# Performance work log

Hardware: AMD Instinct MI355X
Metric: run time of the kernel (lower is better)

The kernel has to match this reference:

```python
import jax, jax.numpy as jnp
import numpy as np

NH = 8  # num_heads


def setup_inputs() -> dict:
    key = jax.random.key(0)
    ks = jax.random.split(key, 6)
    B, H, W, M, C = 4, 32, 32, 21, 32  # M = 1^2 + 2^2 + 4^2 (window_sizes)
    B_ = B * H * W
    hd = C // NH
    s = lambda k, sh: jax.random.normal(k, sh, dtype=jnp.float32) * 0.02
    return {
        'x': jax.random.normal(ks[0], (B_, M, C), dtype=jnp.float32),
        'W_qkv': s(ks[1], (C, 3 * C)),
        'b_qkv': jnp.zeros((3 * C,), jnp.float32),
        'W_proj': s(ks[2], (C, C)),
        'b_proj': jnp.zeros((C,), jnp.float32),
        'W_sq': s(ks[3], (M * hd, 1)),
        'b_sq': jnp.zeros((1,), jnp.float32),
        'W_dw': s(ks[4], (2 * NH, 1, 3, 3)),  # depthwise conv, 2 outputs per head
        'b_dw': jnp.zeros((2 * NH,), jnp.float32),
        'batch_size': B,
        'H': H,
        'W': W,
    }


def reference(x, W_qkv, b_qkv, W_proj, b_proj, W_sq, b_sq, W_dw, b_dw, batch_size, H, W):
    B_, M, C = x.shape
    nh = NH
    hd = C // nh
    N = B_ // batch_size  # = H * W

    # qkv: (B_, M, 3C) -> (3, B, nh, N, M*hd)
    qkv = (x @ W_qkv + b_qkv).reshape(batch_size, N, M, 3, nh, hd)
    qkv = jnp.transpose(qkv, (3, 0, 4, 1, 2, 5)).reshape(3, batch_size, nh, N, M * hd)
    q, k, v = qkv[0], qkv[1], qkv[2]

    scale = N ** -0.5  # qk_scale=None -> (B_//batch_size)**-0.5
    attn = jnp.einsum('bhnd,bhmd->bhnm', q * scale, k)  # (B, nh, N, N)

    # ---- LSPE dynamic relative-position bias ----
    x2 = x.reshape(batch_size, H, W, M, nh, hd)
    x2 = jnp.transpose(x2, (0, 4, 1, 2, 3, 5)).reshape(batch_size, nh, H, W, M * hd)
    x2 = (x2 @ W_sq)[..., 0] + b_sq[0]  # (B, nh, H, W)

    conv = jax.lax.conv_general_dilated(
        x2, W_dw, (1, 1), [(1, 1), (1, 1)],
        dimension_numbers=('NCHW', 'OIHW', 'NCHW'), feature_group_count=nh)
    conv = conv + b_dw[None, :, None, None]  # (B, 2*nh, H, W)

    avg = jnp.mean(x2, axis=(2, 3), keepdims=True)  # adaptive avg pool to 1x1
    mx = jnp.max(x2, axis=(2, 3), keepdims=True)    # adaptive max pool to 1x1
    pooled = jnp.tile(avg + mx, (1, 2, H, W))       # torch .repeat(1,2,H,W)

    y = (conv + pooled).reshape(batch_size, 2, nh, H, W)
    y = jnp.transpose(y, (1, 0, 2, 3, 4))  # (2, B, nh, H, W)
    x_weight = jnp.mean(y[0], axis=0)[:, None]  # (nh, 1, H, W)
    x_proj = jnp.mean(y[1], axis=0)[None]       # (1, nh, H, W)

    # conv_transpose2d(stride=1, pad=0, groups=nh) == full correlation with flipped kernel
    bias = jax.lax.conv_general_dilated(
        x_proj, jnp.flip(x_weight, (-2, -1)), (1, 1),
        [(H - 1, H - 1), (W - 1, W - 1)],
        dimension_numbers=('NCHW', 'OIHW', 'NCHW'), feature_group_count=nh)
    table = bias[0].reshape(nh, -1).T  # ((2H-1)(2W-1), nh)

    coords = jnp.stack(jnp.meshgrid(jnp.arange(H), jnp.arange(W), indexing='ij'))
    coords = coords.reshape(2, -1)                     # (2, N)
    rel = coords[:, :, None] - coords[:, None, :]      # (2, N, N)
    idx = (rel[0] + H - 1) * (2 * W - 1) + (rel[1] + W - 1)  # (N, N)
    rel_bias = jnp.transpose(table[idx], (2, 0, 1))    # (nh, N, N)

    attn = jax.nn.softmax(attn + rel_bias[None], axis=-1)

    out = jnp.einsum('bhnm,bhmd->bhnd', attn, v)       # (B, nh, N, M*hd)
    out = jnp.transpose(out, (0, 2, 1, 3)).reshape(B_, nh, M, hd)
    out = jnp.transpose(out, (0, 2, 1, 3)).reshape(B_, M, C)
    return out @ W_proj + b_proj
```

## Files before the change

kernel.cpp:

```cpp
#include <hip/hip_runtime.h>
#include <math.h>

#define NHEAD 8
#define BATCH 4
#define NN 1024
#define MM 21
#define DD 84
#define DP 96
#define BN (BATCH*NHEAD)
#define NROWS (BATCH*NN*MM)

typedef __attribute__((ext_vector_type(8))) short bf16x8;
typedef __attribute__((ext_vector_type(16))) float f32x16;

__device__ __forceinline__ unsigned short f2bf(float x) {
    union { float f; unsigned int u; } c; c.f = x;
    unsigned int r = (c.u + 0x7FFFu + ((c.u >> 16) & 1u)) >> 16;
    return (unsigned short)r;
}
__device__ __forceinline__ int qxmap(int r, int half) { return (r & 3) + 8*(r >> 2) + 4*half; }


__global__ __launch_bounds__(256)
void qkv_kernel(const float* __restrict__ x, const float* __restrict__ Wq,
                const float* __restrict__ bq, ushort* __restrict__ qf,
                ushort* __restrict__ kf, ushort* __restrict__ vb)
{
    __shared__ ushort wqs[3072];
    __shared__ float bqs[96];
    __shared__ __align__(16) float xs[128*36];
    __shared__ ushort cs[4*3200];
    int t = threadIdx.x;
    int w = t >> 6, lane = t & 63, col = lane & 31, half = lane >> 5;
    int R0 = blockIdx.x * 128;

    for (int i = t; i < 3072; i += 256) wqs[i] = f2bf(Wq[i]);
    if (t < 96) bqs[t] = bq[t];
    for (int i = t; i < 4096; i += 256)
        xs[(i >> 5)*36 + (i & 31)] = x[(size_t)R0*32 + i];
    __syncthreads();

    bf16x8 bw[3][2];
#pragma unroll
    for (int f = 0; f < 3; f++)
#pragma unroll
        for (int c = 0; c < 2; c++) {
            union { bf16x8 v; ushort s[8]; } u;
#pragma unroll
            for (int j = 0; j < 8; j++)
                u.s[j] = wqs[(c*16 + half*8 + j)*96 + f*32 + col];
            bw[f][c] = u.v;
        }
    bf16x8 aw[2];
#pragma unroll
    for (int c = 0; c < 2; c++) {
        const float* xr = xs + (w*32 + col)*36 + c*16 + half*8;
        float4 v0 = *(const float4*)(xr);
        float4 v1 = *(const float4*)(xr + 4);
        union { bf16x8 v; ushort s[8]; } u;
        u.s[0]=f2bf(v0.x); u.s[1]=f2bf(v0.y); u.s[2]=f2bf(v0.z); u.s[3]=f2bf(v0.w);
        u.s[4]=f2bf(v1.x); u.s[5]=f2bf(v1.y); u.s[6]=f2bf(v1.z); u.s[7]=f2bf(v1.w);
        aw[c] = u.v;
    }
    f32x16 acc[3];
#pragma unroll
    for (int f = 0; f < 3; f++) {
#pragma unroll
        for (int r = 0; r < 16; r++) acc[f][r] = 0.f;
#pragma unroll
        for (int c = 0; c < 2; c++)
            acc[f] = __builtin_amdgcn_mfma_f32_32x32x16_bf16(aw[c], bw[f][c], acc[f], 0, 0, 0);
    }
    ushort* myc = cs + w*3200;
#pragma unroll
    for (int f = 0; f < 3; f++) {
        float sc = (f == 0) ? 0.03125f : 1.0f;
        float bb = bqs[f*32 + col];
#pragma unroll
        for (int r = 0; r < 16; r++)
            myc[qxmap(r, half)*100 + f*32 + col] = f2bf((acc[f][r] + bb)*sc);
    }
    __syncthreads();
    int row = lane >> 1, hr = lane & 1;
    int Rr = R0 + w*32 + row;
    int b_ = Rr / 21, m = Rr - b_*21, b = b_ >> 10, n = b_ & 1023;
    size_t fragoff = (size_t)(m >> 2)*512 + ((m >> 1) & 1)*256 + (n & 31)*8 + ((4*m) & 7);
    int nt = n >> 5;
#pragma unroll
    for (int c2 = 0; c2 < 12; c2++) {
        int col4 = hr*48 + c2*4;
        ushort4 v = *(const ushort4*)(myc + row*100 + col4);
        int s = col4 >> 5, hh = (col4 & 31) >> 2;
        if (s == 0)
            *(ushort4*)(qf + (size_t)((b*8 + hh)*32 + nt)*3072 + fragoff) = v;
        else if (s == 1)
            *(ushort4*)(kf + (size_t)((b*8 + hh)*32 + nt)*3072 + fragoff) = v;
        else
            *(ushort4*)(vb + ((size_t)((b*8 + hh)*1024 + n))*DD + m*4) = v;
    }
}

__global__ __launch_bounds__(256)
void vtr_kernel(const ushort* __restrict__ vb, ushort* __restrict__ vf)
{
    __shared__ ushort ld[64*88];
    int t = threadIdx.x;
    int bh = blockIdx.y, n0 = blockIdx.x * 64;
    for (int i = t; i < 1344; i += 256) {
        int r = i/21, p = i - r*21;
        *(ushort4*)(ld + r*88 + p*4) = *(const ushort4*)(vb + ((size_t)bh*NN + n0 + r)*DD + p*4);
    }
    __syncthreads();
    for (int j = t; j < 1344; j += 256) {
        int d = j >> 4, g = j & 15;
        ushort4 wv;
        wv.x = ld[(g*4+0)*88 + d]; wv.y = ld[(g*4+1)*88 + d];
        wv.z = ld[(g*4+2)*88 + d]; wv.w = ld[(g*4+3)*88 + d];
        int nn = n0 + g*4;
        size_t addr = (size_t)(bh*32 + (nn >> 5))*3072 + (d >> 5)*1024
                    + ((nn >> 4) & 1)*512 + ((nn >> 3) & 1)*256 + (d & 31)*8 + (nn & 7);
        *(ushort4*)(vf + addr) = wv;
    }
    if (t < 192) {
        int r = 84 + t/16, p = t & 15;
        int nn = n0 + p*4;
        ushort e = (r == 84) ? (ushort)0x3F80 : (ushort)0;
        size_t addr = (size_t)(bh*32 + (nn >> 5))*3072 + 2*1024
                    + ((nn >> 4) & 1)*512 + ((nn >> 3) & 1)*256 + (r & 31)*8 + (nn & 7);
        *(ushort4*)(vf + addr) = make_ushort4(e, e, e, e);
    }
}

__global__ __launch_bounds__(256)
void x2_kernel(const float* __restrict__ x, const float* __restrict__ Wsq,
               const float* __restrict__ bsq, float* __restrict__ x2,
               unsigned* __restrict__ Mg, ushort* __restrict__ qf,
               ushort* __restrict__ kf)
{
    __shared__ __align__(16) float ws[84];
    int t = threadIdx.x;
    if (t < 84) ws[t] = Wsq[t];
    if (blockIdx.x == 0 && t < 8) Mg[t] = 0u;
    __syncthreads();
    int w = t >> 6, l = t & 63;
    int wid = blockIdx.x*4 + w;
    float bs0 = bsq[0];
    int dd = l & 3;
    for (int rr = 0; rr < 4; rr++) {
        int row = wid*4 + rr;
        int b = row >> 10, n = row & 1023;
        const float* xr = x + (size_t)row*672;
        float acc = 0.f;
#pragma unroll
        for (int p = 0; p < 11; p++) {
            int idx = p*64 + l;
            int m = idx >> 5;
            if (m < 21) acc += xr[idx] * ws[m*4 + dd];
        }
        acc += __shfl_xor(acc, 32);
        acc += __shfl_xor(acc, 1);
        acc += __shfl_xor(acc, 2);
        if ((l & 3) == 0 && l < 32) {
            int h = l >> 2;
            x2[(size_t)(b*8 + h)*1024 + n] = acc + bs0;
        }
        if (l < 48) {
            int h = l / 6, piece = l % 6;
            size_t base = (size_t)((b*8 + h)*32 + (n >> 5))*3072 + 5*512 + (n & 31)*8;
            int pm = piece % 3;
            size_t off = (pm == 0) ? 4 : (pm == 1) ? 256 : 260;
            ushort* dst = (piece < 3) ? qf : kf;
            *(ushort4*)(dst + base + off) = make_ushort4(0,0,0,0);
        }
    }
}

__global__ __launch_bounds__(256)
void pool_kernel(const float* __restrict__ x2, float* __restrict__ spool)
{
    int bh = blockIdx.x;
    int t = threadIdx.x;
    const float* p = x2 + (size_t)bh*NN;
    float s = 0.f, mx = -INFINITY;
    for (int i = t; i < NN; i += 256) { float v = p[i]; s += v; mx = fmaxf(mx, v); }
#pragma unroll
    for (int off = 1; off < 64; off <<= 1) {
        s  += __shfl_xor(s, off);
        mx  = fmaxf(mx, __shfl_xor(mx, off));
    }
    __shared__ float rs[4], rm[4];
    int w = t >> 6;
    if ((t & 63) == 0) { rs[w] = s; rm[w] = mx; }
    __syncthreads();
    if (t == 0) {
        float ss = rs[0]+rs[1]+rs[2]+rs[3];
        float mm = fmaxf(fmaxf(rm[0],rm[1]), fmaxf(rm[2],rm[3]));
        spool[bh] = ss * (1.f/1024.f) + mm;
    }
}

__global__ __launch_bounds__(256)
void lspe_kernel(const float* __restrict__ x2, const float* __restrict__ spool,
                 const float* __restrict__ Wdw, const float* __restrict__ bdw,
                 float* __restrict__ xw, float* __restrict__ xp)
{
    int i = blockIdx.x*256 + threadIdx.x;
    int h = i >> 10;
    int n = i & 1023;
    int y = n >> 5, xx = n & 31;
    int g0 = h >> 1;
    float accW = 0.f, accP = 0.f;
    for (int b = 0; b < 4; b++) {
        float sp = spool[b*8 + h];
        float c0 = bdw[h], c1 = bdw[8 + h];
        const float* a0 = x2 + (size_t)(b*8 + g0)*NN;
        const float* a1 = x2 + (size_t)(b*8 + 4 + g0)*NN;
#pragma unroll
        for (int ky = 0; ky < 3; ky++) {
            int yy = y + ky - 1;
            if (yy < 0 || yy > 31) continue;
#pragma unroll
            for (int kx = 0; kx < 3; kx++) {
                int xc = xx + kx - 1;
                if (xc < 0 || xc > 31) continue;
                c0 += a0[yy*32 + xc] * Wdw[h*9 + ky*3 + kx];
                c1 += a1[yy*32 + xc] * Wdw[(8+h)*9 + ky*3 + kx];
            }
        }
        accW += c0 + sp;
        accP += c1 + sp;
    }
    xw[i] = 0.25f * accW;
    xp[i] = 0.25f * accP;
}

__global__ __launch_bounds__(512)
void bias_kernel(const float* __restrict__ xw, const float* __restrict__ xp,
                 float* __restrict__ btab, unsigned* __restrict__ Mg)
{
    __shared__ float sxw[1024], sxp[1024];
    __shared__ float part[8][64];
    int h = blockIdx.y, oy = blockIdx.x;
    int t = threadIdx.x;
    for (int i = t; i < 1024; i += 512) { sxw[i] = xw[h*1024+i]; sxp[i] = xp[h*1024+i]; }
    __syncthreads();
    int ox = t & 63;
    int aw = t >> 6;
    int alo = max(0, oy-31), ahi = min(31, oy);
    int clo = max(0, ox-31), chi = min(31, ox);
    int cnt = chi - clo + 1;
    float acc0 = 0.f, acc1 = 0.f;
    if (ox < 63) {
        for (int a = alo + aw; a <= ahi; a += 8) {
            const float* prow = sxp + a*32 + clo;
            const float* wrow = sxw + (oy - a)*32 + (ox - clo);
            int k = 0;
            for (; k + 1 < cnt; k += 2) {
                acc0 += prow[k]   * wrow[-k];
                acc1 += prow[k+1] * wrow[-k-1];
            }
            if (k < cnt) acc0 += prow[k] * wrow[-k];
        }
    }
    part[aw][ox] = acc0 + acc1;
    __syncthreads();
    if (t < 64) {
        float acc = 0.f;
#pragma unroll
        for (int j = 0; j < 8; j++) acc += part[j][t];
        unsigned key = 0u;
        if (t < 63) {
            btab[h*3969 + oy*63 + t] = acc;
            unsigned u = __float_as_uint(acc);
            key = (u & 0x80000000u) ? ~u : (u | 0x80000000u);
        }
#pragma unroll
        for (int off = 1; off < 64; off <<= 1) {
            unsigned o = __shfl_xor(key, off);
            key = key > o ? key : o;
        }
        if (t == 0) atomicMax(Mg + h, key);
    }
}

__global__ __launch_bounds__(256, 4)
void attn_kernel(const ushort* __restrict__ qg, const ushort* __restrict__ kg,
                 const ushort* __restrict__ vg, const float* __restrict__ btg,
                 const unsigned* __restrict__ Mg, float* __restrict__ Obuf)
{
    __shared__ float btabS[2016];
    __shared__ float red[2][64*52];
    __shared__ float lred[32];

    int t = threadIdx.x;
    int bid = blockIdx.x;
    int bh = bid & 31, qt = bid >> 5;
    int h = bh & 7, b = bh >> 3;
    int q0 = qt * 32;

    float Mh;
    { unsigned k = Mg[h]; unsigned u = (k & 0x80000000u) ? (k ^ 0x80000000u) : ~k; Mh = __uint_as_float(u); }
    const float* bsrc = btg + h*3969 + qt*63;
    for (int i = t; i < 2016; i += 256) btabS[i] = bsrc[i] - Mh;
    __syncthreads();

    int w = t >> 6, lane = t & 63, col = lane & 31, half = lane >> 5;
    int lofs = half*256 + col*8;

    bf16x8 bq6[6];
    const ushort* qbase = qg + (size_t)(bh*32 + qt)*3072 + lofs;
#pragma unroll
    for (int s = 0; s < 6; s++) bq6[s] = *(const bf16x8*)(qbase + s*512);

    f32x16 of[3];
#pragma unroll
    for (int f = 0; f < 3; f++)
#pragma unroll
        for (int r = 0; r < 16; r++) of[f][r] = 0.f;

    int kx_[16];
#pragma unroll
    for (int r = 0; r < 16; r++) kx_[r] = qxmap(r, half);

    const ushort* kall = kg + (size_t)bh*32*3072 + lofs;
    const ushort* vall = vg + (size_t)bh*32*3072 + lofs;

    bf16x8 akc[6];
    {
        const ushort* kr = kall + (size_t)w*3072;
#pragma unroll
        for (int s = 0; s < 6; s++) akc[s] = *(const bf16x8*)(kr + s*512);
    }

    for (int j = 0; j < 8; j++) {
        int kt = 4*j + w;
        const ushort* vr = vall + (size_t)kt*3072;
        bf16x8 vfr[3][2];
#pragma unroll
        for (int f = 0; f < 3; f++)
#pragma unroll
            for (int c = 0; c < 2; c++)
                vfr[f][c] = *(const bf16x8*)(vr + f*1024 + c*512);

        f32x16 st;
#pragma unroll
        for (int r = 0; r < 16; r++) st[r] = 0.f;
#pragma unroll
        for (int s = 0; s < 6; s++)
            st = __builtin_amdgcn_mfma_f32_32x32x16_bf16(akc[s], bq6[s], st, 0, 0, 0);

        bf16x8 akn[6];
        if (j < 7) {
            const ushort* kr = kall + (size_t)(kt + 4)*3072;
#pragma unroll
            for (int s = 0; s < 6; s++) akn[s] = *(const bf16x8*)(kr + s*512);
        }

        const float* bp = btabS + (31 - kt)*63 + col + 31;
        unsigned P[8];
#pragma unroll
        for (int g = 0; g < 8; g++) {
            float p0 = __expf(st[2*g]   + bp[-kx_[2*g]]);
            float p1 = __expf(st[2*g+1] + bp[-kx_[2*g+1]]);
            unsigned u0 = __float_as_uint(p0) + 0x8000u;
            unsigned u1 = __float_as_uint(p1) + 0x8000u;
            P[g] = (u1 & 0xFFFF0000u) | (u0 >> 16);
        }
        unsigned XP[8];
#pragma unroll
        for (int g = 0; g < 8; g++) XP[g] = (unsigned)__shfl_xor((int)P[g], 32);

        union { bf16x8 v; unsigned u[4]; } f0, f1;
        f0.u[0] = half ? XP[2] : P[0];
        f0.u[1] = half ? XP[3] : P[1];
        f0.u[2] = half ? P[2]  : XP[0];
        f0.u[3] = half ? P[3]  : XP[1];
        f1.u[0] = half ? XP[6] : P[4];
        f1.u[1] = half ? XP[7] : P[5];
        f1.u[2] = half ? P[6]  : XP[4];
        f1.u[3] = half ? P[7]  : XP[5];

#pragma unroll
        for (int f = 0; f < 3; f++) {
            of[f] = __builtin_amdgcn_mfma_f32_32x32x16_bf16(f0.v, vfr[f][0], of[f], 0, 0, 0);
            of[f] = __builtin_amdgcn_mfma_f32_32x32x16_bf16(f1.v, vfr[f][1], of[f], 0, 0, 0);
        }
        if (j < 7) {
#pragma unroll
            for (int s = 0; s < 6; s++) akc[s] = akn[s];
        }
    }

    __syncthreads();
    if (w == 1 || w == 3) {
        float* dst = red[w >> 1] + lane*52;
#pragma unroll
        for (int f = 0; f < 3; f++)
#pragma unroll
            for (int r = 0; r < 16; r++) dst[f*16 + r] = of[f][r];
    }
    __syncthreads();
    if (w == 0 || w == 2) {
        const float* src = red[w >> 1] + lane*52;
#pragma unroll
        for (int f = 0; f < 3; f++)
#pragma unroll
            for (int r = 0; r < 16; r++) of[f][r] += src[f*16 + r];
    }
    __syncthreads();
    if (w == 2) {
        float* dst = red[0] + lane*52;
#pragma unroll
        for (int f = 0; f < 3; f++)
#pragma unroll
            for (int r = 0; r < 16; r++) dst[f*16 + r] = of[f][r];
    }
    __syncthreads();
    if (w == 0) {
        const float* src = red[0] + lane*52;
#pragma unroll
        for (int f = 0; f < 3; f++)
#pragma unroll
            for (int r = 0; r < 16; r++) of[f][r] += src[f*16 + r];
        if (col == 20) {
#pragma unroll
            for (int r = 0; r < 16; r++) lred[qxmap(r, half)] = of[2][r];
        }
    }
    __syncthreads();
    if (w == 0) {
        float linv[16];
#pragma unroll
        for (int r = 0; r < 16; r++) linv[r] = 1.0f / lred[qxmap(r, half)];
#pragma unroll
        for (int f = 0; f < 3; f++) {
            int d = f*32 + col;
            if (d < DD) {
                int m = d >> 2, dd2 = d & 3;
#pragma unroll
                for (int r = 0; r < 16; r++) {
                    int q = qxmap(r, half);
                    size_t R = ((size_t)(b*NN + q0 + q))*21 + m;
                    Obuf[R*32 + h*4 + dd2] = of[f][r] * linv[r];
                }
            }
        }
    }
}

__global__ __launch_bounds__(256)
void proj_kernel(const float* __restrict__ Obuf, const float* __restrict__ Wp,
                 const float* __restrict__ bp, float* __restrict__ out)
{
    __shared__ ushort wps[1024];
    __shared__ float bps[32];
    __shared__ __align__(16) float os[128*36];
    int t = threadIdx.x;
    int w = t >> 6, lane = t & 63, col = lane & 31, half = lane >> 5;
    int R0 = blockIdx.x * 128;
    for (int i = t; i < 1024; i += 256) wps[i] = f2bf(Wp[i]);
    if (t < 32) bps[t] = bp[t];
    for (int i = t; i < 4096; i += 256)
        os[(i >> 5)*36 + (i & 31)] = Obuf[(size_t)R0*32 + i];
    __syncthreads();

    bf16x8 bw[2];
#pragma unroll
    for (int c = 0; c < 2; c++) {
        union { bf16x8 v; ushort s[8]; } u;
#pragma unroll
        for (int j = 0; j < 8; j++)
            u.s[j] = wps[(c*16 + half*8 + j)*32 + col];
        bw[c] = u.v;
    }
    bf16x8 aw[2];
#pragma unroll
    for (int c = 0; c < 2; c++) {
        const float* orr = os + (w*32 + col)*36 + c*16 + half*8;
        float4 v0 = *(const float4*)(orr);
        float4 v1 = *(const float4*)(orr + 4);
        union { bf16x8 v; ushort s[8]; } u;
        u.s[0]=f2bf(v0.x); u.s[1]=f2bf(v0.y); u.s[2]=f2bf(v0.z); u.s[3]=f2bf(v0.w);
        u.s[4]=f2bf(v1.x); u.s[5]=f2bf(v1.y); u.s[6]=f2bf(v1.z); u.s[7]=f2bf(v1.w);
        aw[c] = u.v;
    }
    f32x16 acc;
#pragma unroll
    for (int r = 0; r < 16; r++) acc[r] = 0.f;
#pragma unroll
    for (int c = 0; c < 2; c++)
        acc = __builtin_amdgcn_mfma_f32_32x32x16_bf16(aw[c], bw[c], acc, 0, 0, 0);
    float bb = bps[col];
#pragma unroll
    for (int r = 0; r < 16; r++)
        out[(size_t)(R0 + w*32 + qxmap(r, half))*32 + col] = acc[r] + bb;
}

extern "C" void kernel_launch(void* const* d_in, const int* in_sizes, int n_in,
                              void* d_out, int out_size, void* d_ws, size_t ws_size,
                              hipStream_t stream)
{
    const float* x     = (const float*)d_in[0];
    const float* Wqkv  = (const float*)d_in[1];
    const float* bqkv  = (const float*)d_in[2];
    const float* Wproj = (const float*)d_in[3];
    const float* bproj = (const float*)d_in[4];
    const float* Wsq   = (const float*)d_in[5];
    const float* bsq   = (const float*)d_in[6];
    const float* Wdw   = (const float*)d_in[7];
    const float* bdw   = (const float*)d_in[8];

    const size_t QP = (size_t)BN * NN * DP;
    const size_t VB = (size_t)BN * NN * DD;
    ushort* qf   = (ushort*)d_ws;
    ushort* kf   = qf + QP;
    ushort* vb   = kf + QP;
    ushort* vf   = vb + VB;
    float* Obuf  = (float*)(vf + QP);
    float* x2    = Obuf + VB;
    float* spool = x2 + 32768;
    float* xw    = spool + 32;
    float* xp    = xw + 8192;
    float* btab  = xp + 8192;
    unsigned* Mg = (unsigned*)(btab + 3969*8);
    float* out   = (float*)d_out;

    qkv_kernel <<<NROWS/128, 256, 0, stream>>>(x, Wqkv, bqkv, qf, kf, vb);
    vtr_kernel <<<dim3(16,32),256, 0, stream>>>(vb, vf);
    x2_kernel  <<<256,        256, 0, stream>>>(x, Wsq, bsq, x2, Mg, qf, kf);
    pool_kernel<<<32,         256, 0, stream>>>(x2, spool);
    lspe_kernel<<<32,         256, 0, stream>>>(x2, spool, Wdw, bdw, xw, xp);
    bias_kernel<<<dim3(63,8), 512, 0, stream>>>(xw, xp, btab, Mg);
    attn_kernel<<<1024,       256, 0, stream>>>(qf, kf, vf, btab, Mg, Obuf);
    proj_kernel<<<NROWS/128,  256, 0, stream>>>(Obuf, Wproj, bproj, out);
}
```

Measured before the change: 157.3 us.

## Merge independent pre-attention kernels into two horizontally fused launches

```diff
diff --git a/kernel.cpp b/kernel.cpp
--- a/kernel.cpp
+++ b/kernel.cpp
@@ -22,216 +22,203 @@
 
 
 __global__ __launch_bounds__(256)
-void qkv_kernel(const float* __restrict__ x, const float* __restrict__ Wq,
-                const float* __restrict__ bq, ushort* __restrict__ qf,
-                ushort* __restrict__ kf, ushort* __restrict__ vb)
+void l1_kernel(const float* __restrict__ x, const float* __restrict__ Wq,
+               const float* __restrict__ bq, const float* __restrict__ Wsq,
+               const float* __restrict__ bsq, ushort* __restrict__ qf,
+               ushort* __restrict__ kf, ushort* __restrict__ vb,
+               float* __restrict__ x2, unsigned* __restrict__ Mg)
 {
-    __shared__ ushort wqs[3072];
-    __shared__ float bqs[96];
-    __shared__ __align__(16) float xs[128*36];
-    __shared__ ushort cs[4*3200];
     int t = threadIdx.x;
     int w = t >> 6, lane = t & 63, col = lane & 31, half = lane >> 5;
-    int R0 = blockIdx.x * 128;
-
-    for (int i = t; i < 3072; i += 256) wqs[i] = f2bf(Wq[i]);
-    if (t < 96) bqs[t] = bq[t];
-    for (int i = t; i < 4096; i += 256)
-        xs[(i >> 5)*36 + (i & 31)] = x[(size_t)R0*32 + i];
-    __syncthreads();
-
-    bf16x8 bw[3][2];
-#pragma unroll
-    for (int f = 0; f < 3; f++)
+
+    if (blockIdx.x < 672) {
+        __shared__ ushort wqs[3072];
+        __shared__ float bqs[96];
+        __shared__ __align__(16) float xs[128*36];
+        __shared__ ushort cs[4*3200];
+        int R0 = blockIdx.x * 128;
+
+        for (int i = t; i < 3072; i += 256) wqs[i] = f2bf(Wq[i]);
+        if (t < 96) bqs[t] = bq[t];
+        for (int i = t; i < 4096; i += 256)
+            xs[(i >> 5)*36 + (i & 31)] = x[(size_t)R0*32 + i];
+        __syncthreads();
+
+        bf16x8 bw[3][2];
+#pragma unroll
+        for (int f = 0; f < 3; f++)
+#pragma unroll
+            for (int c = 0; c < 2; c++) {
+                union { bf16x8 v; ushort s[8]; } u;
+#pragma unroll
+                for (int j = 0; j < 8; j++)
+                    u.s[j] = wqs[(c*16 + half*8 + j)*96 + f*32 + col];
+                bw[f][c] = u.v;
+            }
+        bf16x8 aw[2];
 #pragma unroll
         for (int c = 0; c < 2; c++) {
+            const float* xr = xs + (w*32 + col)*36 + c*16 + half*8;
+            float4 v0 = *(const float4*)(xr);
+            float4 v1 = *(const float4*)(xr + 4);
             union { bf16x8 v; ushort s[8]; } u;
-#pragma unroll
-            for (int j = 0; j < 8; j++)
-                u.s[j] = wqs[(c*16 + half*8 + j)*96 + f*32 + col];
-            bw[f][c] = u.v;
-        }
-    bf16x8 aw[2];
-#pragma unroll
-    for (int c = 0; c < 2; c++) {
-        const float* xr = xs + (w*32 + col)*36 + c*16 + half*8;
-        float4 v0 = *(const float4*)(xr);
-        float4 v1 = *(const float4*)(xr + 4);
-        union { bf16x8 v; ushort s[8]; } u;
-        u.s[0]=f2bf(v0.x); u.s[1]=f2bf(v0.y); u.s[2]=f2bf(v0.z); u.s[3]=f2bf(v0.w);
-        u.s[4]=f2bf(v1.x); u.s[5]=f2bf(v1.y); u.s[6]=f2bf(v1.z); u.s[7]=f2bf(v1.w);
-        aw[c] = u.v;
-    }
-    f32x16 acc[3];
-#pragma unroll
-    for (int f = 0; f < 3; f++) {
-#pragma unroll
-        for (int r = 0; r < 16; r++) acc[f][r] = 0.f;
-#pragma unroll
-        for (int c = 0; c < 2; c++)
-            acc[f] = __builtin_amdgcn_mfma_f32_32x32x16_bf16(aw[c], bw[f][c], acc[f], 0, 0, 0);
-    }
-    ushort* myc = cs + w*3200;
-#pragma unroll
-    for (int f = 0; f < 3; f++) {
-        float sc = (f == 0) ? 0.03125f : 1.0f;
-        float bb = bqs[f*32 + col];
-#pragma unroll
-        for (int r = 0; r < 16; r++)
-            myc[qxmap(r, half)*100 + f*32 + col] = f2bf((acc[f][r] + bb)*sc);
-    }
-    __syncthreads();
-    int row = lane >> 1, hr = lane & 1;
-    int Rr = R0 + w*32 + row;
-    int b_ = Rr / 21, m = Rr - b_*21, b = b_ >> 10, n = b_ & 1023;
-    size_t fragoff = (size_t)(m >> 2)*512 + ((m >> 1) & 1)*256 + (n & 31)*8 + ((4*m) & 7);
-    int nt = n >> 5;
-#pragma unroll
-    for (int c2 = 0; c2 < 12; c2++) {
-        int col4 = hr*48 + c2*4;
-        ushort4 v = *(const ushort4*)(myc + row*100 + col4);
-        int s = col4 >> 5, hh = (col4 & 31) >> 2;
-        if (s == 0)
-            *(ushort4*)(qf + (size_t)((b*8 + hh)*32 + nt)*3072 + fragoff) = v;
-        else if (s == 1)
-            *(ushort4*)(kf + (size_t)((b*8 + hh)*32 + nt)*3072 + fragoff) = v;
-        else
-            *(ushort4*)(vb + ((size_t)((b*8 + hh)*1024 + n))*DD + m*4) = v;
+            u.s[0]=f2bf(v0.x); u.s[1]=f2bf(v0.y); u.s[2]=f2bf(v0.z); u.s[3]=f2bf(v0.w);
+            u.s[4]=f2bf(v1.x); u.s[5]=f2bf(v1.y); u.s[6]=f2bf(v1.z); u.s[7]=f2bf(v1.w);
+            aw[c] = u.v;
+        }
+        f32x16 acc[3];
+#pragma unroll
+        for (int f = 0; f < 3; f++) {
+#pragma unroll
+            for (int r = 0; r < 16; r++) acc[f][r] = 0.f;
+#pragma unroll
+            for (int c = 0; c < 2; c++)
+                acc[f] = __builtin_amdgcn_mfma_f32_32x32x16_bf16(aw[c], bw[f][c], acc[f], 0, 0, 0);
+        }
+        ushort* myc = cs + w*3200;
+#pragma unroll
+        for (int f = 0; f < 3; f++) {
+            float sc = (f == 0) ? 0.03125f : 1.0f;
+            float bb = bqs[f*32 + col];
+#pragma unroll
+            for (int r = 0; r < 16; r++)
+                myc[qxmap(r, half)*100 + f*32 + col] = f2bf((acc[f][r] + bb)*sc);
+        }
+        __syncthreads();
+        int row = lane >> 1, hr = lane & 1;
+        int Rr = R0 + w*32 + row;
+        int b_ = Rr / 21, m = Rr - b_*21, b = b_ >> 10, n = b_ & 1023;
+        size_t fragoff = (size_t)(m >> 2)*512 + ((m >> 1) & 1)*256 + (n & 31)*8 + ((4*m) & 7);
+        int nt = n >> 5;
+#pragma unroll
+        for (int c2 = 0; c2 < 12; c2++) {
+            int col4 = hr*48 + c2*4;
+            ushort4 v = *(const ushort4*)(myc + row*100 + col4);
+            int s = col4 >> 5, hh = (col4 & 31) >> 2;
+            if (s == 0)
+                *(ushort4*)(qf + (size_t)((b*8 + hh)*32 + nt)*3072 + fragoff) = v;
+            else if (s == 1)
+                *(ushort4*)(kf + (size_t)((b*8 + hh)*32 + nt)*3072 + fragoff) = v;
+            else
+                *(ushort4*)(vb + ((size_t)((b*8 + hh)*1024 + n))*DD + m*4) = v;
+        }
+    } else {
+        __shared__ __align__(16) float ws[84];
+        int bx = blockIdx.x - 672;
+        if (t < 84) ws[t] = Wsq[t];
+        if (bx == 0 && t < 8) Mg[t] = 0u;
+        __syncthreads();
+        int wid = bx*4 + w;
+        float bs0 = bsq[0];
+        int dd = lane & 3;
+        for (int rr = 0; rr < 16; rr++) {
+            int rowi = wid*16 + rr;
+            int b = rowi >> 10, n = rowi & 1023;
+            const float* xr = x + (size_t)rowi*672;
+            float acc = 0.f;
+#pragma unroll
+            for (int p = 0; p < 11; p++) {
+                int idx = p*64 + lane;
+                int m = idx >> 5;
+                if (m < 21) acc += xr[idx] * ws[m*4 + dd];
+            }
+            acc += __shfl_xor(acc, 32);
+            acc += __shfl_xor(acc, 1);
+            acc += __shfl_xor(acc, 2);
+            if ((lane & 3) == 0 && lane < 32) {
+                int h = lane >> 2;
+                x2[(size_t)(b*8 + h)*1024 + n] = acc + bs0;
+            }
+            if (lane < 48) {
+                int h = lane / 6, piece = lane % 6;
+                size_t base = (size_t)((b*8 + h)*32 + (n >> 5))*3072 + 5*512 + (n & 31)*8;
+                int pm = piece % 3;
+                size_t off = (pm == 0) ? 4 : (pm == 1) ? 256 : 260;
+                ushort* dst = (piece < 3) ? qf : kf;
+                *(ushort4*)(dst + base + off) = make_ushort4(0,0,0,0);
+            }
+        }
     }
 }
 
 __global__ __launch_bounds__(256)
-void vtr_kernel(const ushort* __restrict__ vb, ushort* __restrict__ vf)
+void l2_kernel(const ushort* __restrict__ vb, ushort* __restrict__ vf,
+               const float* __restrict__ x2, const float* __restrict__ Wdw,
+               const float* __restrict__ bdw, float* __restrict__ xw,
+               float* __restrict__ xp)
 {
-    __shared__ ushort ld[64*88];
     int t = threadIdx.x;
-    int bh = blockIdx.y, n0 = blockIdx.x * 64;
-    for (int i = t; i < 1344; i += 256) {
-        int r = i/21, p = i - r*21;
-        *(ushort4*)(ld + r*88 + p*4) = *(const ushort4*)(vb + ((size_t)bh*NN + n0 + r)*DD + p*4);
-    }
-    __syncthreads();
-    for (int j = t; j < 1344; j += 256) {
-        int d = j >> 4, g = j & 15;
-        ushort4 wv;
-        wv.x = ld[(g*4+0)*88 + d]; wv.y = ld[(g*4+1)*88 + d];
-        wv.z = ld[(g*4+2)*88 + d]; wv.w = ld[(g*4+3)*88 + d];
-        int nn = n0 + g*4;
-        size_t addr = (size_t)(bh*32 + (nn >> 5))*3072 + (d >> 5)*1024
-                    + ((nn >> 4) & 1)*512 + ((nn >> 3) & 1)*256 + (d & 31)*8 + (nn & 7);
-        *(ushort4*)(vf + addr) = wv;
-    }
-    if (t < 192) {
-        int r = 84 + t/16, p = t & 15;
-        int nn = n0 + p*4;
-        ushort e = (r == 84) ? (ushort)0x3F80 : (ushort)0;
-        size_t addr = (size_t)(bh*32 + (nn >> 5))*3072 + 2*1024
-                    + ((nn >> 4) & 1)*512 + ((nn >> 3) & 1)*256 + (r & 31)*8 + (nn & 7);
-        *(ushort4*)(vf + addr) = make_ushort4(e, e, e, e);
-    }
-}
-
-__global__ __launch_bounds__(256)
-void x2_kernel(const float* __restrict__ x, const float* __restrict__ Wsq,
-               const float* __restrict__ bsq, float* __restrict__ x2,
-               unsigned* __restrict__ Mg, ushort* __restrict__ qf,
-               ushort* __restrict__ kf)
-{
-    __shared__ __align__(16) float ws[84];
-    int t = threadIdx.x;
-    if (t < 84) ws[t] = Wsq[t];
-    if (blockIdx.x == 0 && t < 8) Mg[t] = 0u;
-    __syncthreads();
-    int w = t >> 6, l = t & 63;
-    int wid = blockIdx.x*4 + w;
-    float bs0 = bsq[0];
-    int dd = l & 3;
-    for (int rr = 0; rr < 4; rr++) {
-        int row = wid*4 + rr;
-        int b = row >> 10, n = row & 1023;
-        const float* xr = x + (size_t)row*672;
-        float acc = 0.f;
-#pragma unroll
-        for (int p = 0; p < 11; p++) {
-            int idx = p*64 + l;
-            int m = idx >> 5;
-            if (m < 21) acc += xr[idx] * ws[m*4 + dd];
-        }
-        acc += __shfl_xor(acc, 32);
-        acc += __shfl_xor(acc, 1);
-        acc += __shfl_xor(acc, 2);
-        if ((l & 3) == 0 && l < 32) {
-            int h = l >> 2;
-            x2[(size_t)(b*8 + h)*1024 + n] = acc + bs0;
-        }
-        if (l < 48) {
-            int h = l / 6, piece = l % 6;
-            size_t base = (size_t)((b*8 + h)*32 + (n >> 5))*3072 + 5*512 + (n & 31)*8;
-            int pm = piece % 3;
-            size_t off = (pm == 0) ? 4 : (pm == 1) ? 256 : 260;
-            ushort* dst = (piece < 3) ? qf : kf;
-            *(ushort4*)(dst + base + off) = make_ushort4(0,0,0,0);
-        }
-    }
-}
-
-__global__ __launch_bounds__(256)
-void pool_kernel(const float* __restrict__ x2, float* __restrict__ spool)
-{
-    int bh = blockIdx.x;
-    int t = threadIdx.x;
-    const float* p = x2 + (size_t)bh*NN;
-    float s = 0.f, mx = -INFINITY;
-    for (int i = t; i < NN; i += 256) { float v = p[i]; s += v; mx = fmaxf(mx, v); }
-#pragma unroll
-    for (int off = 1; off < 64; off <<= 1) {
-        s  += __shfl_xor(s, off);
-        mx  = fmaxf(mx, __shfl_xor(mx, off));
-    }
-    __shared__ float rs[4], rm[4];
-    int w = t >> 6;
-    if ((t & 63) == 0) { rs[w] = s; rm[w] = mx; }
-    __syncthreads();
-    if (t == 0) {
-        float ss = rs[0]+rs[1]+rs[2]+rs[3];
-        float mm = fmaxf(fmaxf(rm[0],rm[1]), fmaxf(rm[2],rm[3]));
-        spool[bh] = ss * (1.f/1024.f) + mm;
-    }
-}
-
-__global__ __launch_bounds__(256)
-void lspe_kernel(const float* __restrict__ x2, const float* __restrict__ spool,
-                 const float* __restrict__ Wdw, const float* __restrict__ bdw,
-                 float* __restrict__ xw, float* __restrict__ xp)
-{
-    int i = blockIdx.x*256 + threadIdx.x;
-    int h = i >> 10;
-    int n = i & 1023;
-    int y = n >> 5, xx = n & 31;
-    int g0 = h >> 1;
-    float accW = 0.f, accP = 0.f;
-    for (int b = 0; b < 4; b++) {
-        float sp = spool[b*8 + h];
-        float c0 = bdw[h], c1 = bdw[8 + h];
-        const float* a0 = x2 + (size_t)(b*8 + g0)*NN;
-        const float* a1 = x2 + (size_t)(b*8 + 4 + g0)*NN;
-#pragma unroll
-        for (int ky = 0; ky < 3; ky++) {
-            int yy = y + ky - 1;
-            if (yy < 0 || yy > 31) continue;
-#pragma unroll
-            for (int kx = 0; kx < 3; kx++) {
-                int xc = xx + kx - 1;
-                if (xc < 0 || xc > 31) continue;
-                c0 += a0[yy*32 + xc] * Wdw[h*9 + ky*3 + kx];
-                c1 += a1[yy*32 + xc] * Wdw[(8+h)*9 + ky*3 + kx];
-            }
-        }
-        accW += c0 + sp;
-        accP += c1 + sp;
-    }
-    xw[i] = 0.25f * accW;
-    xp[i] = 0.25f * accP;
+    if (blockIdx.x < 512) {
+        __shared__ ushort ld[64*88];
+        int bh = blockIdx.x >> 4, n0 = (blockIdx.x & 15) * 64;
+        for (int i = t; i < 1344; i += 256) {
+            int r = i/21, p = i - r*21;
+            *(ushort4*)(ld + r*88 + p*4) = *(const ushort4*)(vb + ((size_t)bh*NN + n0 + r)*DD + p*4);
+        }
+        __syncthreads();
+        for (int j = t; j < 1344; j += 256) {
+            int d = j >> 4, g = j & 15;
+            ushort4 wv;
+            wv.x = ld[(g*4+0)*88 + d]; wv.y = ld[(g*4+1)*88 + d];
+            wv.z = ld[(g*4+2)*88 + d]; wv.w = ld[(g*4+3)*88 + d];
+            int nn = n0 + g*4;
+            size_t addr = (size_t)(bh*32 + (nn >> 5))*3072 + (d >> 5)*1024
+                        + ((nn >> 4) & 1)*512 + ((nn >> 3) & 1)*256 + (d & 31)*8 + (nn & 7);
+            *(ushort4*)(vf + addr) = wv;
+        }
+        if (t < 192) {
+            int r = 84 + t/16, p = t & 15;
+            int nn = n0 + p*4;
+            ushort e = (r == 84) ? (ushort)0x3F80 : (ushort)0;
+            size_t addr = (size_t)(bh*32 + (nn >> 5))*3072 + 2*1024
+                        + ((nn >> 4) & 1)*512 + ((nn >> 3) & 1)*256 + (r & 31)*8 + (nn & 7);
+            *(ushort4*)(vf + addr) = make_ushort4(e, e, e, e);
+        }
+    } else {
+        __shared__ float sp[4];
+        int idx = blockIdx.x - 512;
+        int w = t >> 6, lane = t & 63;
+        int i = idx*256 + t;
+        int h = i >> 10;
+        {
+            const float* p = x2 + (size_t)(w*8 + h)*NN;
+            float s = 0.f, mx = -INFINITY;
+            for (int k = lane; k < NN; k += 64) { float v = p[k]; s += v; mx = fmaxf(mx, v); }
+#pragma unroll
+            for (int off = 1; off < 64; off <<= 1) {
+                s  += __shfl_xor(s, off);
+                mx  = fmaxf(mx, __shfl_xor(mx, off));
+            }
+            if (lane == 0) sp[w] = s * (1.f/1024.f) + mx;
+        }
+        __syncthreads();
+        int n = i & 1023;
+        int y = n >> 5, xx = n & 31;
+        int g0 = h >> 1;
+        float accW = 0.f, accP = 0.f;
+        for (int b = 0; b < 4; b++) {
+            float spl = sp[b];
+            float c0 = bdw[h], c1 = bdw[8 + h];
+            const float* a0 = x2 + (size_t)(b*8 + g0)*NN;
+            const float* a1 = x2 + (size_t)(b*8 + 4 + g0)*NN;
+#pragma unroll
+            for (int ky = 0; ky < 3; ky++) {
+                int yy = y + ky - 1;
+                if (yy < 0 || yy > 31) continue;
+#pragma unroll
+                for (int kx = 0; kx < 3; kx++) {
+                    int xc = xx + kx - 1;
+                    if (xc < 0 || xc > 31) continue;
+                    c0 += a0[yy*32 + xc] * Wdw[h*9 + ky*3 + kx];
+                    c1 += a1[yy*32 + xc] * Wdw[(8+h)*9 + ky*3 + kx];
+                }
+            }
+            accW += c0 + spl;
+            accP += c1 + spl;
+        }
+        xw[i] = 0.25f * accW;
+        xp[i] = 0.25f * accP;
+    }
 }
 
 __global__ __launch_bounds__(512)
@@ -518,18 +505,14 @@
     ushort* vf   = vb + VB;
     float* Obuf  = (float*)(vf + QP);
     float* x2    = Obuf + VB;
-    float* spool = x2 + 32768;
-    float* xw    = spool + 32;
+    float* xw    = x2 + 32768;
     float* xp    = xw + 8192;
     float* btab  = xp + 8192;
     unsigned* Mg = (unsigned*)(btab + 3969*8);
     float* out   = (float*)d_out;
 
-    qkv_kernel <<<NROWS/128, 256, 0, stream>>>(x, Wqkv, bqkv, qf, kf, vb);
-    vtr_kernel <<<dim3(16,32),256, 0, stream>>>(vb, vf);
-    x2_kernel  <<<256,        256, 0, stream>>>(x, Wsq, bsq, x2, Mg, qf, kf);
-    pool_kernel<<<32,         256, 0, stream>>>(x2, spool);
-    lspe_kernel<<<32,         256, 0, stream>>>(x2, spool, Wdw, bdw, xw, xp);
+    l1_kernel  <<<736,        256, 0, stream>>>(x, Wqkv, bqkv, Wsq, bsq, qf, kf, vb, x2, Mg);
+    l2_kernel  <<<544,        256, 0, stream>>>(vb, vf, x2, Wdw, bdw, xw, xp);
     bias_kernel<<<dim3(63,8), 512, 0, stream>>>(xw, xp, btab, Mg);
     attn_kernel<<<1024,       256, 0, stream>>>(qf, kf, vf, btab, Mg, Obuf);
     proj_kernel<<<NROWS/128,  256, 0, stream>>>(Obuf, Wproj, bproj, out);
```

New measurement: 153.2 us. 1.03x faster.
